# Kernel tuning notes

Measured on AMD Instinct MI355X. Metric: run time of the kernel, lower is better.

Reference implementation:

```python
import jax, jax.numpy as jnp
import numpy as np

NUM_GRAPHS = 128
N_NODES = 50000
N_EDGES = 400000
EMB = 384
L = 5
BN_EPS = 1e-5


def _bn(h, gamma, beta):
    # training-mode BatchNorm1d over the node/edge dim (biased variance, like torch)
    m = h.mean(axis=0)
    v = h.var(axis=0)
    return gamma * (h - m) * jax.lax.rsqrt(v + BN_EPS) + beta


def setup_inputs() -> dict:
    key = jax.random.key(0)
    ks = jax.random.split(key, 16)
    batch = jnp.sort(jax.random.randint(ks[0], (N_NODES,), 0, NUM_GRAPHS))
    x = jax.random.randint(ks[1], (N_NODES, 9), 0, 64)
    edge_index = jax.random.randint(ks[2], (2, N_EDGES), 0, N_NODES)
    edge_attr = jax.random.randint(ks[3], (N_EDGES, 3), 0, 8)
    s = 0.05
    atom_emb = jax.random.normal(ks[4], (9, 64, EMB), jnp.float32) * s
    bond_emb = jax.random.normal(ks[5], (3, 8, EMB), jnp.float32) * s
    # per-layer GINE MLP params, stacked over layers
    W1 = jax.random.normal(ks[6], (L, EMB, 2 * EMB), jnp.float32) * (1.0 / np.sqrt(EMB))
    b1 = jnp.zeros((L, 2 * EMB), jnp.float32)
    g1 = jnp.ones((L, 2 * EMB), jnp.float32)
    be1 = jnp.zeros((L, 2 * EMB), jnp.float32)
    W2 = jax.random.normal(ks[7], (L, 2 * EMB, EMB), jnp.float32) * (1.0 / np.sqrt(2 * EMB))
    b2 = jnp.zeros((L, EMB), jnp.float32)
    # outer per-layer BatchNorm params
    gbn = jnp.ones((L, EMB), jnp.float32)
    bbn = jnp.zeros((L, EMB), jnp.float32)
    return {"batch": batch, "x": x, "edge_index": edge_index, "edge_attr": edge_attr,
            "atom_emb": atom_emb, "bond_emb": bond_emb,
            "W1": W1, "b1": b1, "g1": g1, "be1": be1,
            "W2": W2, "b2": b2, "gbn": gbn, "bbn": bbn}


def reference(batch, x, edge_index, edge_attr, atom_emb, bond_emb,
              W1, b1, g1, be1, W2, b2, gbn, bbn):
    # AtomEncoder / BondEncoder: sum of per-column embedding lookups
    h = atom_emb[jnp.arange(9), x].sum(axis=1)          # [N, EMB]
    e = bond_emb[jnp.arange(3), edge_attr].sum(axis=1)  # [E, EMB]
    src, dst = edge_index[0], edge_index[1]
    for i in range(W1.shape[0]):
        # GINEConv: sum_j relu(x_j + e_ij)  (edge_weight defaults to ones)
        msg = jax.nn.relu(h[src] + e)                                   # [E, EMB]
        agg = jax.ops.segment_sum(msg, dst, num_segments=N_NODES)      # [N, EMB]
        z = h + agg                                                     # (1+eps)*x_i + agg, eps=0
        # MLP: Linear -> BN -> ReLU -> Linear
        z = z @ W1[i] + b1[i]
        z = jax.nn.relu(_bn(z, g1[i], be1[i]))
        z = z @ W2[i] + b2[i]
        # outer BN + ReLU (drop_ratio = 0.0)
        h = jax.nn.relu(_bn(z, gbn[i], bbn[i]))
    # standard pooling: global_add_pool
    graph_emb = jax.ops.segment_sum(h, batch, num_segments=NUM_GRAPHS)  # [G, EMB]
    return graph_emb, h
```

## Files before the change

### kernel.cpp

```cpp
#include <hip/hip_runtime.h>
#include <stdint.h>

#define NN 50000
#define NE 400000
#define EMB 384
#define NH 768
#define NL 5

typedef __bf16 bf16x8_t __attribute__((ext_vector_type(8)));
typedef float  f32x4_t  __attribute__((ext_vector_type(4)));

__device__ __forceinline__ float bflo(uint32_t u){ union{uint32_t u;float f;} v; v.u = u<<16; return v.f; }
__device__ __forceinline__ float bfhi(uint32_t u){ union{uint32_t u;float f;} v; v.u = u & 0xffff0000u; return v.f; }
__device__ __forceinline__ uint16_t f2bf(float f){
  union{float f;uint32_t u;} v; v.f=f;
  uint32_t r = v.u + 0x7fffu + ((v.u>>16)&1u);
  return (uint16_t)(r>>16);
}
__device__ __forceinline__ uint32_t bfpack2(float a, float b){
  return (uint32_t)f2bf(a) | ((uint32_t)f2bf(b)<<16);
}

__global__ void hist_kernel(const int* __restrict__ dst, int* __restrict__ count){
  int i = blockIdx.x*256 + threadIdx.x;
  if (i < NE) atomicAdd(&count[dst[i]], 1);
}
__global__ void scan_block_sum(const int* __restrict__ count, int* __restrict__ bsum, int n){
  __shared__ int s[256];
  int i = blockIdx.x*256 + threadIdx.x;
  s[threadIdx.x] = (i<n) ? count[i] : 0;
  __syncthreads();
  for (int st=128; st>0; st>>=1){
    if (threadIdx.x < st) s[threadIdx.x] += s[threadIdx.x+st];
    __syncthreads();
  }
  if (threadIdx.x==0) bsum[blockIdx.x] = s[0];
}
__global__ void scan_excl_small(int* __restrict__ bsum, int nb){
  __shared__ int s[256];
  int t = threadIdx.x;
  int v = (t<nb) ? bsum[t] : 0;
  s[t] = v;
  __syncthreads();
  for (int st=1; st<256; st<<=1){
    int u = (t>=st) ? s[t-st] : 0;
    __syncthreads();
    s[t] += u;
    __syncthreads();
  }
  if (t<nb) bsum[t] = s[t] - v;
}
__global__ void scan_final(const int* __restrict__ count, const int* __restrict__ bsum,
                           int* __restrict__ rowptr, int* __restrict__ cursor, int n){
  __shared__ int s[256];
  int t = threadIdx.x;
  int i = blockIdx.x*256 + t;
  int v = (i<n) ? count[i] : 0;
  s[t] = v;
  __syncthreads();
  for (int st=1; st<256; st<<=1){
    int u = (t>=st) ? s[t-st] : 0;
    __syncthreads();
    s[t] += u;
    __syncthreads();
  }
  int off = bsum[blockIdx.x] + s[t] - v;
  if (i < n){
    rowptr[i] = off; cursor[i] = off;
    if (i == n-1) rowptr[n] = off + v;
  }
}
__global__ void scatter_kernel(const int* __restrict__ dst, const int* __restrict__ src,
                               const int* __restrict__ eattr, int* __restrict__ cursor,
                               int* __restrict__ csr_src, int* __restrict__ csr_code){
  int e = blockIdx.x*256 + threadIdx.x;
  if (e < NE){
    int p = atomicAdd(&cursor[dst[e]], 1);
    csr_src[p] = src[e];
    csr_code[p] = eattr[e*3] | (eattr[e*3+1]<<3) | (eattr[e*3+2]<<6);
  }
}

__global__ void build_bond(const float* __restrict__ bemb, uint16_t* __restrict__ bt){
  const int code = blockIdx.x;
  const int t0 = code&7, t1=(code>>3)&7, t2=code>>6;
  const int c = threadIdx.x;
  const float2 a = ((const float2*)(bemb + (size_t)( 0+t0)*EMB))[c];
  const float2 b = ((const float2*)(bemb + (size_t)( 8+t1)*EMB))[c];
  const float2 d = ((const float2*)(bemb + (size_t)(16+t2)*EMB))[c];
  ((uint32_t*)(bt + (size_t)code*EMB))[c] = bfpack2(a.x+b.x+d.x, a.y+b.y+d.y);
}

__global__ void transpose_w(const float* __restrict__ in, uint16_t* __restrict__ outp,
                            int R, int Cc){
  __shared__ float tile[32][33];
  const size_t lo = (size_t)blockIdx.z * R * Cc;
  int cb = blockIdx.x*32, rb = blockIdx.y*32;
  int r = rb + threadIdx.y, c = cb + threadIdx.x;
  if (r < R && c < Cc) tile[threadIdx.y][threadIdx.x] = in[lo + (size_t)r*Cc + c];
  __syncthreads();
  int orr = cb + threadIdx.y, occ = rb + threadIdx.x;
  if (orr < Cc && occ < R) outp[lo + (size_t)orr*R + occ] = f2bf(tile[threadIdx.x][threadIdx.y]);
}

__global__ __launch_bounds__(256) void atom_encode(
    const int* __restrict__ x, const float* __restrict__ aemb,
    uint16_t* __restrict__ h){
  const int w = threadIdx.x >> 6, lane = threadIdx.x & 63;
  const int i = blockIdx.x*4 + w;
  if (i >= NN) return;
  float a0=0,a1=0,a2=0,a3=0,a4=0,a5=0;
  #pragma unroll
  for (int k=0;k<9;k++){
    const int idx = x[i*9+k];
    const float2* p = (const float2*)(aemb + ((size_t)(k*64+idx))*EMB) + lane*3;
    float2 u0=p[0], u1=p[1], u2=p[2];
    a0+=u0.x; a1+=u0.y; a2+=u1.x; a3+=u1.y; a4+=u2.x; a5+=u2.y;
  }
  uint32_t* hp = (uint32_t*)(h + (size_t)i*EMB) + lane*3;
  hp[0]=bfpack2(a0,a1); hp[1]=bfpack2(a2,a3); hp[2]=bfpack2(a4,a5);
}

template<int BNREL>
__global__ __launch_bounds__(256) void agg_kernel(
    const uint16_t* __restrict__ in, const uint16_t* __restrict__ bondt,
    const float* __restrict__ scale, const float* __restrict__ shift,
    const int* __restrict__ rowptr, const int* __restrict__ csr_src,
    const int* __restrict__ csr_code, uint16_t* __restrict__ za){
  const int w = threadIdx.x >> 6, lane = threadIdx.x & 63;
  const int i = blockIdx.x*4 + w;
  if (i >= NN) return;

  float sc0=0,sc1=0,sc2=0,sc3=0,sc4=0,sc5=0, sh0=0,sh1=0,sh2=0,sh3=0,sh4=0,sh5=0;
  if (BNREL){
    const int c = lane*6;
    sc0=scale[c]; sc1=scale[c+1]; sc2=scale[c+2]; sc3=scale[c+3]; sc4=scale[c+4]; sc5=scale[c+5];
    sh0=shift[c]; sh1=shift[c+1]; sh2=shift[c+2]; sh3=shift[c+3]; sh4=shift[c+4]; sh5=shift[c+5];
  }

  const uint32_t* hs = (const uint32_t*)(in + (size_t)i*EMB) + lane*3;
  uint32_t s0=hs[0], s1=hs[1], s2=hs[2];
  float a0,a1,a2,a3,a4,a5;
  if (BNREL){
    a0 = fmaxf(bflo(s0)*sc0+sh0, 0.f); a1 = fmaxf(bfhi(s0)*sc1+sh1, 0.f);
    a2 = fmaxf(bflo(s1)*sc2+sh2, 0.f); a3 = fmaxf(bfhi(s1)*sc3+sh3, 0.f);
    a4 = fmaxf(bflo(s2)*sc4+sh4, 0.f); a5 = fmaxf(bfhi(s2)*sc5+sh5, 0.f);
  } else {
    a0 = bflo(s0); a1 = bfhi(s0); a2 = bflo(s1); a3 = bfhi(s1); a4 = bflo(s2); a5 = bfhi(s2);
  }

  const int rs = rowptr[i], re = rowptr[i+1];
  int k = rs;
  for (; k + 4 <= re; k += 4){
    int sj[4], cj[4];
    #pragma unroll
    for (int j=0;j<4;j++){ sj[j]=csr_src[k+j]; cj[j]=csr_code[k+j]; }
    uint32_t u[4][3], b[4][3];
    #pragma unroll
    for (int j=0;j<4;j++){
      const uint32_t* hp = (const uint32_t*)(in + (size_t)sj[j]*EMB) + lane*3;
      u[j][0]=hp[0]; u[j][1]=hp[1]; u[j][2]=hp[2];
      const uint32_t* bp = (const uint32_t*)(bondt + (size_t)cj[j]*EMB) + lane*3;
      b[j][0]=bp[0]; b[j][1]=bp[1]; b[j][2]=bp[2];
    }
    #pragma unroll
    for (int j=0;j<4;j++){
      float v0,v1,v2,v3,v4,v5;
      if (BNREL){
        v0 = fmaxf(bflo(u[j][0])*sc0+sh0, 0.f); v1 = fmaxf(bfhi(u[j][0])*sc1+sh1, 0.f);
        v2 = fmaxf(bflo(u[j][1])*sc2+sh2, 0.f); v3 = fmaxf(bfhi(u[j][1])*sc3+sh3, 0.f);
        v4 = fmaxf(bflo(u[j][2])*sc4+sh4, 0.f); v5 = fmaxf(bfhi(u[j][2])*sc5+sh5, 0.f);
      } else {
        v0=bflo(u[j][0]); v1=bfhi(u[j][0]); v2=bflo(u[j][1]);
        v3=bfhi(u[j][1]); v4=bflo(u[j][2]); v5=bfhi(u[j][2]);
      }
      a0 += fmaxf(v0+bflo(b[j][0]), 0.f); a1 += fmaxf(v1+bfhi(b[j][0]), 0.f);
      a2 += fmaxf(v2+bflo(b[j][1]), 0.f); a3 += fmaxf(v3+bfhi(b[j][1]), 0.f);
      a4 += fmaxf(v4+bflo(b[j][2]), 0.f); a5 += fmaxf(v5+bfhi(b[j][2]), 0.f);
    }
  }
  for (; k < re; k++){
    const int s = csr_src[k];
    const int code = csr_code[k];
    const uint32_t* hp = (const uint32_t*)(in + (size_t)s*EMB) + lane*3;
    uint32_t u0=hp[0], u1=hp[1], u2=hp[2];
    const uint32_t* bp = (const uint32_t*)(bondt + (size_t)code*EMB) + lane*3;
    uint32_t b0=bp[0], b1=bp[1], b2=bp[2];
    float v0,v1,v2,v3,v4,v5;
    if (BNREL){
      v0 = fmaxf(bflo(u0)*sc0+sh0, 0.f); v1 = fmaxf(bfhi(u0)*sc1+sh1, 0.f);
      v2 = fmaxf(bflo(u1)*sc2+sh2, 0.f); v3 = fmaxf(bfhi(u1)*sc3+sh3, 0.f);
      v4 = fmaxf(bflo(u2)*sc4+sh4, 0.f); v5 = fmaxf(bfhi(u2)*sc5+sh5, 0.f);
    } else {
      v0=bflo(u0); v1=bfhi(u0); v2=bflo(u1); v3=bfhi(u1); v4=bflo(u2); v5=bfhi(u2);
    }
    a0 += fmaxf(v0+bflo(b0), 0.f); a1 += fmaxf(v1+bfhi(b0), 0.f);
    a2 += fmaxf(v2+bflo(b1), 0.f); a3 += fmaxf(v3+bfhi(b1), 0.f);
    a4 += fmaxf(v4+bflo(b2), 0.f); a5 += fmaxf(v5+bfhi(b2), 0.f);
  }

  uint32_t* zp = (uint32_t*)(za + (size_t)i*EMB) + lane*3;
  zp[0] = bfpack2(a0,a1);
  zp[1] = bfpack2(a2,a3);
  zp[2] = bfpack2(a4,a5);
}

template<int BNA>
__global__ __launch_bounds__(256) void gemm_bt(
    const uint16_t* __restrict__ A, const uint16_t* __restrict__ Bt,
    const float* __restrict__ bias, const float* __restrict__ scA,
    const float* __restrict__ shA, uint16_t* __restrict__ C,
    float* __restrict__ stats, int M, int N, int K, int nbr){
  __shared__ __align__(16) uint16_t As[128*32];
  __shared__ __align__(16) uint16_t Bs[128*32];
  __shared__ float sAs[BNA ? NH : 1];
  __shared__ float hAs[BNA ? NH : 1];
  __shared__ float csum[128];
  __shared__ float csq[128];

  const int tid = threadIdx.x;
  const int nbc = N >> 7;
  const int xcd = blockIdx.x & 7;
  const int slot = blockIdx.x >> 3;
  const int bcol = slot % nbc;
  const int brow = (slot / nbc)*8 + xcd;
  if (brow >= nbr) return;
  const int rowbase = brow << 7;

  const int lane = tid & 63;
  const int w = tid >> 6;
  const int wm = w >> 1, wn = w & 1;
  const int quad = lane >> 4, l16 = lane & 15;

  const int s0 = tid, s1 = 256 + tid;
  const int kq0 = s0 >> 7, r0 = s0 & 127;
  const int kq1 = s1 >> 7, r1 = s1 & 127;
  int gra0 = rowbase + r0; if (gra0 >= M) gra0 = M-1;
  int gra1 = rowbase + r1; if (gra1 >= M) gra1 = M-1;
  const int pb0 = bcol*128 + (r0 & 64) + ((r0 & 15) << 2) + ((r0 >> 4) & 3);
  const int pb1 = bcol*128 + (r1 & 64) + ((r1 & 15) << 2) + ((r1 >> 4) & 3);

  const uint16_t* gA0 = A + (size_t)gra0*K + kq0*8;
  const uint16_t* gA1 = A + (size_t)gra1*K + kq1*8;
  const uint16_t* gB0 = Bt + (size_t)pb0*K + kq0*8;
  const uint16_t* gB1 = Bt + (size_t)pb1*K + kq1*8;

  uint4 pa0 = *(const uint4*)gA0;
  uint4 pa1 = *(const uint4*)gA1;
  uint4 pb0r = *(const uint4*)gB0;
  uint4 pb1r = *(const uint4*)gB1;
  uint4 qa0 = *(const uint4*)(gA0 + 32);
  uint4 qa1 = *(const uint4*)(gA1 + 32);
  uint4 qb0r = *(const uint4*)(gB0 + 32);
  uint4 qb1r = *(const uint4*)(gB1 + 32);

  if (BNA){
    for (int i = tid; i < K; i += 256){ sAs[i] = scA[i]; hAs[i] = shA[i]; }
    __syncthreads();
  }

  f32x4_t acc[4][4];
  #pragma unroll
  for (int mi=0;mi<4;mi++)
    #pragma unroll
    for (int ni=0;ni<4;ni++)
      acc[mi][ni] = (f32x4_t){0.f,0.f,0.f,0.f};

  for (int k0 = 0; k0 < K; k0 += 64){
    if (!BNA){
      *(uint4*)&As[s0*8] = pa0;
      *(uint4*)&As[s1*8] = pa1;
    } else {
      uint32_t in0[4] = {pa0.x,pa0.y,pa0.z,pa0.w};
      uint32_t in1[4] = {pa1.x,pa1.y,pa1.z,pa1.w};
      uint32_t o0[4], o1[4];
      const int kb0 = k0 + kq0*8, kb1 = k0 + kq1*8;
      #pragma unroll
      for (int j=0;j<4;j++){
        float x0 = fmaxf(bflo(in0[j])*sAs[kb0+2*j  ]+hAs[kb0+2*j  ], 0.f);
        float x1 = fmaxf(bfhi(in0[j])*sAs[kb0+2*j+1]+hAs[kb0+2*j+1], 0.f);
        o0[j] = bfpack2(x0,x1);
        float y0 = fmaxf(bflo(in1[j])*sAs[kb1+2*j  ]+hAs[kb1+2*j  ], 0.f);
        float y1 = fmaxf(bfhi(in1[j])*sAs[kb1+2*j+1]+hAs[kb1+2*j+1], 0.f);
        o1[j] = bfpack2(y0,y1);
      }
      *(uint4*)&As[s0*8] = make_uint4(o0[0],o0[1],o0[2],o0[3]);
      *(uint4*)&As[s1*8] = make_uint4(o1[0],o1[1],o1[2],o1[3]);
    }
    *(uint4*)&Bs[s0*8] = pb0r;
    *(uint4*)&Bs[s1*8] = pb1r;
    __syncthreads();

    if (k0 + 64 < K){
      const int kn = k0 + 64;
      pa0 = *(const uint4*)(gA0 + kn);
      pa1 = *(const uint4*)(gA1 + kn);
      pb0r = *(const uint4*)(gB0 + kn);
      pb1r = *(const uint4*)(gB1 + kn);
    }

    {
      bf16x8_t fa[4], fb[4];
      #pragma unroll
      for (int mi=0;mi<4;mi++)
        fa[mi] = *(const bf16x8_t*)&As[(quad*128 + wm*64 + mi*16 + l16)*8];
      #pragma unroll
      for (int ni=0;ni<4;ni++)
        fb[ni] = *(const bf16x8_t*)&Bs[(quad*128 + wn*64 + ni*16 + l16)*8];
      #pragma unroll
      for (int mi=0;mi<4;mi++)
        #pragma unroll
        for (int ni=0;ni<4;ni++)
          acc[mi][ni] = __builtin_amdgcn_mfma_f32_16x16x32_bf16(fa[mi], fb[ni], acc[mi][ni], 0,0,0);
    }
    __syncthreads();

    if (!BNA){
      *(uint4*)&As[s0*8] = qa0;
      *(uint4*)&As[s1*8] = qa1;
    } else {
      uint32_t in0[4] = {qa0.x,qa0.y,qa0.z,qa0.w};
      uint32_t in1[4] = {qa1.x,qa1.y,qa1.z,qa1.w};
      uint32_t o0[4], o1[4];
      const int kb0 = k0 + 32 + kq0*8, kb1 = k0 + 32 + kq1*8;
      #pragma unroll
      for (int j=0;j<4;j++){
        float x0 = fmaxf(bflo(in0[j])*sAs[kb0+2*j  ]+hAs[kb0+2*j  ], 0.f);
        float x1 = fmaxf(bfhi(in0[j])*sAs[kb0+2*j+1]+hAs[kb0+2*j+1], 0.f);
        o0[j] = bfpack2(x0,x1);
        float y0 = fmaxf(bflo(in1[j])*sAs[kb1+2*j  ]+hAs[kb1+2*j  ], 0.f);
        float y1 = fmaxf(bfhi(in1[j])*sAs[kb1+2*j+1]+hAs[kb1+2*j+1], 0.f);
        o1[j] = bfpack2(y0,y1);
      }
      *(uint4*)&As[s0*8] = make_uint4(o0[0],o0[1],o0[2],o0[3]);
      *(uint4*)&As[s1*8] = make_uint4(o1[0],o1[1],o1[2],o1[3]);
    }
    *(uint4*)&Bs[s0*8] = qb0r;
    *(uint4*)&Bs[s1*8] = qb1r;
    __syncthreads();

    if (k0 + 96 < K){
      const int kn = k0 + 96;
      qa0 = *(const uint4*)(gA0 + kn);
      qa1 = *(const uint4*)(gA1 + kn);
      qb0r = *(const uint4*)(gB0 + kn);
      qb1r = *(const uint4*)(gB1 + kn);
    }

    {
      bf16x8_t fa[4], fb[4];
      #pragma unroll
      for (int mi=0;mi<4;mi++)
        fa[mi] = *(const bf16x8_t*)&As[(quad*128 + wm*64 + mi*16 + l16)*8];
      #pragma unroll
      for (int ni=0;ni<4;ni++)
        fb[ni] = *(const bf16x8_t*)&Bs[(quad*128 + wn*64 + ni*16 + l16)*8];
      #pragma unroll
      for (int mi=0;mi<4;mi++)
        #pragma unroll
        for (int ni=0;ni<4;ni++)
          acc[mi][ni] = __builtin_amdgcn_mfma_f32_16x16x32_bf16(fa[mi], fb[ni], acc[mi][ni], 0,0,0);
    }
    __syncthreads();
  }

  if (tid < 128){ csum[tid]=0.f; csq[tid]=0.f; }
  __syncthreads();

  const int lcol = wn*64 + l16*4;
  const int colbase = bcol*128 + lcol;
  float bv[4], ssum[4] = {0,0,0,0}, sq[4] = {0,0,0,0};
  #pragma unroll
  for (int ni=0;ni<4;ni++) bv[ni] = bias[colbase + ni];

  #pragma unroll
  for (int mi=0;mi<4;mi++){
    #pragma unroll
    for (int r=0;r<4;r++){
      const int grow = rowbase + wm*64 + mi*16 + quad*4 + r;
      if (grow < M){
        float v0 = acc[mi][0][r] + bv[0];
        float v1 = acc[mi][1][r] + bv[1];
        float v2 = acc[mi][2][r] + bv[2];
        float v3 = acc[mi][3][r] + bv[3];
        uint2 pk = make_uint2(bfpack2(v0,v1), bfpack2(v2,v3));
        *(uint2*)(C + (size_t)grow*N + colbase) = pk;
        ssum[0]+=v0; ssum[1]+=v1; ssum[2]+=v2; ssum[3]+=v3;
        sq[0]+=v0*v0; sq[1]+=v1*v1; sq[2]+=v2*v2; sq[3]+=v3*v3;
      }
    }
  }
  #pragma unroll
  for (int ni=0;ni<4;ni++){
    ssum[ni] += __shfl_xor(ssum[ni], 16); ssum[ni] += __shfl_xor(ssum[ni], 32);
    sq[ni]   += __shfl_xor(sq[ni],   16); sq[ni]   += __shfl_xor(sq[ni],   32);
  }
  if (quad == 0){
    #pragma unroll
    for (int ni=0;ni<4;ni++){
      atomicAdd(&csum[lcol + ni], ssum[ni]);
      atomicAdd(&csq [lcol + ni], sq[ni]);
    }
  }
  __syncthreads();
  if (tid < 128){
    atomicAdd(&stats[bcol*128 + tid], csum[tid]);
    atomicAdd(&stats[N + bcol*128 + tid], csq[tid]);
  }
}

__global__ void bn_finalize(float* __restrict__ stats, const float* __restrict__ gamma,
                            const float* __restrict__ beta, float* __restrict__ scale,
                            float* __restrict__ shift, int n, float invM){
  int c = blockIdx.x*256 + threadIdx.x;
  if (c < n){
    float mean = stats[c]*invM;
    float var  = stats[n+c]*invM - mean*mean;
    float sc = gamma[c] * rsqrtf(var + 1e-5f);
    scale[c] = sc;
    shift[c] = beta[c] - mean*sc;
    stats[c] = 0.f;
    stats[n+c] = 0.f;
  }
}

__global__ void bn_relu_final(const uint16_t* __restrict__ u, const float* __restrict__ scale,
                              const float* __restrict__ shift, float* __restrict__ hf){
  int i = blockIdx.x*256 + threadIdx.x;
  const int total2 = NN*EMB/2;
  if (i >= total2) return;
  uint32_t v = ((const uint32_t*)u)[i];
  int c = (i*2) % EMB;
  float f0 = fmaxf(bflo(v)*scale[c  ] + shift[c  ], 0.f);
  float f1 = fmaxf(bfhi(v)*scale[c+1] + shift[c+1], 0.f);
  ((float2*)hf)[i] = make_float2(f0, f1);
}

__global__ void pool_kernel(const float* __restrict__ h, const int* __restrict__ batch,
                            float* __restrict__ pool){
  __shared__ int bs[64];
  int c = threadIdx.x;
  int n0 = blockIdx.x*64;
  if (c < 64){ int i = n0 + c; bs[c] = (i < NN) ? batch[i] : -1; }
  __syncthreads();
  float sum = 0.f; int cur = -1;
  for (int tt=0; tt<64; tt++){
    int i = n0 + tt;
    if (i >= NN) break;
    int g = bs[tt];
    float v = h[(size_t)i*EMB + c];
    if (g != cur){
      if (cur >= 0) atomicAdd(&pool[(size_t)cur*EMB + c], sum);
      cur = g; sum = v;
    } else sum += v;
  }
  if (cur >= 0) atomicAdd(&pool[(size_t)cur*EMB + c], sum);
}
__global__ void pool_to_out(const float* __restrict__ pool, float* __restrict__ outp){
  int i = blockIdx.x*256 + threadIdx.x;
  if (i < 128*EMB) outp[i] = pool[i];
}

extern "C" void kernel_launch(void* const* d_in, const int* in_sizes, int n_in,
                              void* d_out, int out_size, void* d_ws, size_t ws_size,
                              hipStream_t stream){
  (void)in_sizes; (void)n_in; (void)out_size; (void)ws_size;
  const int* batch = (const int*)d_in[0];
  const int* x     = (const int*)d_in[1];
  const int* eidx  = (const int*)d_in[2];
  const int* eattr = (const int*)d_in[3];
  const float* aemb = (const float*)d_in[4];
  const float* bemb = (const float*)d_in[5];
  const float* W1 = (const float*)d_in[6];
  const float* b1 = (const float*)d_in[7];
  const float* g1 = (const float*)d_in[8];
  const float* be1= (const float*)d_in[9];
  const float* W2 = (const float*)d_in[10];
  const float* b2 = (const float*)d_in[11];
  const float* gbn= (const float*)d_in[12];
  const float* bbn= (const float*)d_in[13];
  float* out = (float*)d_out;

  char* base = (char*)d_ws;
  size_t off = 0;
  auto alloc = [&](size_t bytes) -> void* {
    void* p = base + off;
    off = (off + bytes + 255) & ~(size_t)255;
    return p;
  };
  uint16_t* za   = (uint16_t*)alloc((size_t)NN*EMB*2);
  uint16_t* zm   = (uint16_t*)alloc((size_t)NN*EMB*2);
  uint16_t* t    = (uint16_t*)alloc((size_t)NN*NH*2);
  uint16_t* W1t  = (uint16_t*)alloc((size_t)NL*NH*EMB*2);
  uint16_t* W2t  = (uint16_t*)alloc((size_t)NL*EMB*NH*2);
  uint16_t* bondt= (uint16_t*)alloc((size_t)512*EMB*2);
  float* stats1  = (float*)alloc(NH*2*4);
  float* stats2  = (float*)alloc(EMB*2*4);
  float* scale1  = (float*)alloc(NH*4);
  float* shift1  = (float*)alloc(NH*4);
  float* scale2  = (float*)alloc(EMB*4);
  float* shift2  = (float*)alloc(EMB*4);
  float* pool    = (float*)alloc(128*EMB*4);
  int* count   = (int*)alloc((size_t)NN*4);
  int* rowptr  = (int*)alloc((size_t)(NN+1)*4);
  int* cursor  = (int*)alloc((size_t)NN*4);
  int* bsum    = (int*)alloc(256*4);
  int* csr_src = (int*)alloc((size_t)NE*4);
  int* csr_code= (int*)alloc((size_t)NE*4);

  const int* esrc = eidx;
  const int* edst = eidx + NE;
  const int nsb = (NN + 255)/256;

  hipMemsetAsync(count, 0, (size_t)NN*4, stream);
  hist_kernel<<<(NE+255)/256, 256, 0, stream>>>(edst, count);
  scan_block_sum<<<nsb, 256, 0, stream>>>(count, bsum, NN);
  scan_excl_small<<<1, 256, 0, stream>>>(bsum, nsb);
  scan_final<<<nsb, 256, 0, stream>>>(count, bsum, rowptr, cursor, NN);
  scatter_kernel<<<(NE+255)/256, 256, 0, stream>>>(edst, esrc, eattr, cursor, csr_src, csr_code);

  build_bond<<<512, 192, 0, stream>>>(bemb, bondt);
  transpose_w<<<dim3(NH/32, EMB/32, NL), dim3(32,32), 0, stream>>>(W1, W1t, EMB, NH);
  transpose_w<<<dim3(EMB/32, NH/32, NL), dim3(32,32), 0, stream>>>(W2, W2t, NH, EMB);

  atom_encode<<<NN/4, 256, 0, stream>>>(x, aemb, zm);
  hipMemsetAsync(pool, 0, (size_t)128*EMB*4, stream);
  hipMemsetAsync(stats1, 0, (size_t)(6144 + 3072), stream);

  const int nbr = (NN + 127)/128;
  const int nbrr = ((nbr + 7)/8)*8;
  const int g1blocks = nbrr*(NH/128);
  const int g2blocks = nbrr*(EMB/128);
  for (int l = 0; l < NL; l++){
    if (l == 0)
      agg_kernel<0><<<NN/4, 256, 0, stream>>>(zm, bondt, nullptr, nullptr,
                                              rowptr, csr_src, csr_code, za);
    else
      agg_kernel<1><<<NN/4, 256, 0, stream>>>(zm, bondt, scale2, shift2,
                                              rowptr, csr_src, csr_code, za);
    gemm_bt<0><<<g1blocks, 256, 0, stream>>>(
        za, W1t + (size_t)l*NH*EMB, b1 + l*NH, nullptr, nullptr, t, stats1, NN, NH, EMB, nbr);
    bn_finalize<<<(NH+255)/256, 256, 0, stream>>>(stats1, g1 + l*NH, be1 + l*NH,
                                                  scale1, shift1, NH, 1.0f/NN);
    gemm_bt<1><<<g2blocks, 256, 0, stream>>>(
        t, W2t + (size_t)l*EMB*NH, b2 + l*EMB, scale1, shift1, zm, stats2, NN, EMB, NH, nbr);
    bn_finalize<<<(EMB+255)/256, 256, 0, stream>>>(stats2, gbn + l*EMB, bbn + l*EMB,
                                                   scale2, shift2, EMB, 1.0f/NN);
  }
  bn_relu_final<<<(NN*EMB/2 + 255)/256, 256, 0, stream>>>(zm, scale2, shift2, out + 128*EMB);
  pool_kernel<<<(NN+63)/64, 384, 0, stream>>>(out + 128*EMB, batch, pool);
  pool_to_out<<<(128*EMB+255)/256, 256, 0, stream>>>(pool, out);
}
```

Before: 1.302 ms.

## Double-buffer GEMM LDS tiles and load via direct global-to-LDS DMA

The GEMM main loop now uses two LDS buffers for A and B. It uses global_load_lds to stream B tiles, and A tiles when no BN prologue is needed, straight into the next buffer while MFMAs run on the current one. This removes the register staging round trip and one of the two barriers per k-step. The BN-fused A path still goes through registers and is written into the alternate buffer. The change doubles LDS use, which may reduce occupancy. It also depends on the direct-to-LDS loads being complete by the barrier, with no explicit wait on vmcnt.

```diff
diff --git a/kernel.cpp b/kernel.cpp
--- a/kernel.cpp
+++ b/kernel.cpp
@@ -19,6 +19,13 @@
 }
 __device__ __forceinline__ uint32_t bfpack2(float a, float b){
   return (uint32_t)f2bf(a) | ((uint32_t)f2bf(b)<<16);
+}
+
+__device__ __forceinline__ void gld16(uint16_t* ldsp, const uint16_t* gp){
+  __builtin_amdgcn_global_load_lds(
+      (const __attribute__((address_space(1))) uint32_t*)gp,
+      (__attribute__((address_space(3))) uint32_t*)ldsp,
+      16, 0, 0);
 }
 
 __global__ void hist_kernel(const int* __restrict__ dst, int* __restrict__ count){
@@ -211,8 +218,8 @@
     const float* __restrict__ bias, const float* __restrict__ scA,
     const float* __restrict__ shA, uint16_t* __restrict__ C,
     float* __restrict__ stats, int M, int N, int K, int nbr){
-  __shared__ __align__(16) uint16_t As[128*32];
-  __shared__ __align__(16) uint16_t Bs[128*32];
+  __shared__ __align__(16) uint16_t As[2][128*32];
+  __shared__ __align__(16) uint16_t Bs[2][128*32];
   __shared__ float sAs[BNA ? NH : 1];
   __shared__ float hAs[BNA ? NH : 1];
   __shared__ float csum[128];
@@ -245,20 +252,6 @@
   const uint16_t* gB0 = Bt + (size_t)pb0*K + kq0*8;
   const uint16_t* gB1 = Bt + (size_t)pb1*K + kq1*8;
 
-  uint4 pa0 = *(const uint4*)gA0;
-  uint4 pa1 = *(const uint4*)gA1;
-  uint4 pb0r = *(const uint4*)gB0;
-  uint4 pb1r = *(const uint4*)gB1;
-  uint4 qa0 = *(const uint4*)(gA0 + 32);
-  uint4 qa1 = *(const uint4*)(gA1 + 32);
-  uint4 qb0r = *(const uint4*)(gB0 + 32);
-  uint4 qb1r = *(const uint4*)(gB1 + 32);
-
-  if (BNA){
-    for (int i = tid; i < K; i += 256){ sAs[i] = scA[i]; hAs[i] = shA[i]; }
-    __syncthreads();
-  }
-
   f32x4_t acc[4][4];
   #pragma unroll
   for (int mi=0;mi<4;mi++)
@@ -266,102 +259,94 @@
     for (int ni=0;ni<4;ni++)
       acc[mi][ni] = (f32x4_t){0.f,0.f,0.f,0.f};
 
-  for (int k0 = 0; k0 < K; k0 += 64){
-    if (!BNA){
-      *(uint4*)&As[s0*8] = pa0;
-      *(uint4*)&As[s1*8] = pa1;
-    } else {
-      uint32_t in0[4] = {pa0.x,pa0.y,pa0.z,pa0.w};
-      uint32_t in1[4] = {pa1.x,pa1.y,pa1.z,pa1.w};
-      uint32_t o0[4], o1[4];
-      const int kb0 = k0 + kq0*8, kb1 = k0 + kq1*8;
-      #pragma unroll
-      for (int j=0;j<4;j++){
-        float x0 = fmaxf(bflo(in0[j])*sAs[kb0+2*j  ]+hAs[kb0+2*j  ], 0.f);
-        float x1 = fmaxf(bfhi(in0[j])*sAs[kb0+2*j+1]+hAs[kb0+2*j+1], 0.f);
-        o0[j] = bfpack2(x0,x1);
-        float y0 = fmaxf(bflo(in1[j])*sAs[kb1+2*j  ]+hAs[kb1+2*j  ], 0.f);
-        float y1 = fmaxf(bfhi(in1[j])*sAs[kb1+2*j+1]+hAs[kb1+2*j+1], 0.f);
-        o1[j] = bfpack2(y0,y1);
-      }
-      *(uint4*)&As[s0*8] = make_uint4(o0[0],o0[1],o0[2],o0[3]);
-      *(uint4*)&As[s1*8] = make_uint4(o1[0],o1[1],o1[2],o1[3]);
-    }
-    *(uint4*)&Bs[s0*8] = pb0r;
-    *(uint4*)&Bs[s1*8] = pb1r;
-    __syncthreads();
-
-    if (k0 + 64 < K){
-      const int kn = k0 + 64;
-      pa0 = *(const uint4*)(gA0 + kn);
-      pa1 = *(const uint4*)(gA1 + kn);
-      pb0r = *(const uint4*)(gB0 + kn);
-      pb1r = *(const uint4*)(gB1 + kn);
-    }
-
-    {
-      bf16x8_t fa[4], fb[4];
-      #pragma unroll
-      for (int mi=0;mi<4;mi++)
-        fa[mi] = *(const bf16x8_t*)&As[(quad*128 + wm*64 + mi*16 + l16)*8];
+  auto stageB = [&](int buf, int kk){
+    gld16(&Bs[buf][s0*8], gB0 + kk);
+    gld16(&Bs[buf][s1*8], gB1 + kk);
+  };
+  auto stageA_dma = [&](int buf, int kk){
+    gld16(&As[buf][s0*8], gA0 + kk);
+    gld16(&As[buf][s1*8], gA1 + kk);
+  };
+  auto stageA_bn = [&](int buf, int kk, uint4 va, uint4 vb){
+    uint32_t in0[4] = {va.x,va.y,va.z,va.w};
+    uint32_t in1[4] = {vb.x,vb.y,vb.z,vb.w};
+    uint32_t o0[4], o1[4];
+    const int kb0 = kk + kq0*8, kb1 = kk + kq1*8;
+    #pragma unroll
+    for (int j=0;j<4;j++){
+      float x0 = fmaxf(bflo(in0[j])*sAs[kb0+2*j  ]+hAs[kb0+2*j  ], 0.f);
+      float x1 = fmaxf(bfhi(in0[j])*sAs[kb0+2*j+1]+hAs[kb0+2*j+1], 0.f);
+      o0[j] = bfpack2(x0,x1);
+      float y0 = fmaxf(bflo(in1[j])*sAs[kb1+2*j  ]+hAs[kb1+2*j  ], 0.f);
+      float y1 = fmaxf(bfhi(in1[j])*sAs[kb1+2*j+1]+hAs[kb1+2*j+1], 0.f);
+      o1[j] = bfpack2(y0,y1);
+    }
+    *(uint4*)&As[buf][s0*8] = make_uint4(o0[0],o0[1],o0[2],o0[3]);
+    *(uint4*)&As[buf][s1*8] = make_uint4(o1[0],o1[1],o1[2],o1[3]);
+  };
+  auto compute = [&](int buf){
+    bf16x8_t fa[4], fb[4];
+    #pragma unroll
+    for (int mi=0;mi<4;mi++)
+      fa[mi] = *(const bf16x8_t*)&As[buf][(quad*128 + wm*64 + mi*16 + l16)*8];
+    #pragma unroll
+    for (int ni=0;ni<4;ni++)
+      fb[ni] = *(const bf16x8_t*)&Bs[buf][(quad*128 + wn*64 + ni*16 + l16)*8];
+    #pragma unroll
+    for (int mi=0;mi<4;mi++)
       #pragma unroll
       for (int ni=0;ni<4;ni++)
-        fb[ni] = *(const bf16x8_t*)&Bs[(quad*128 + wn*64 + ni*16 + l16)*8];
-      #pragma unroll
-      for (int mi=0;mi<4;mi++)
-        #pragma unroll
-        for (int ni=0;ni<4;ni++)
-          acc[mi][ni] = __builtin_amdgcn_mfma_f32_16x16x32_bf16(fa[mi], fb[ni], acc[mi][ni], 0,0,0);
-    }
+        acc[mi][ni] = __builtin_amdgcn_mfma_f32_16x16x32_bf16(fa[mi], fb[ni], acc[mi][ni], 0,0,0);
+  };
+
+  const int nk = K >> 5;
+
+  uint4 pa0{}, pa1{}, qa0{}, qa1{};
+  if (BNA){
+    for (int i = tid; i < K; i += 256){ sAs[i] = scA[i]; hAs[i] = shA[i]; }
+    pa0 = *(const uint4*)(gA0);      pa1 = *(const uint4*)(gA1);
+    qa0 = *(const uint4*)(gA0 + 32); qa1 = *(const uint4*)(gA1 + 32);
     __syncthreads();
-
-    if (!BNA){
-      *(uint4*)&As[s0*8] = qa0;
-      *(uint4*)&As[s1*8] = qa1;
-    } else {
-      uint32_t in0[4] = {qa0.x,qa0.y,qa0.z,qa0.w};
-      uint32_t in1[4] = {qa1.x,qa1.y,qa1.z,qa1.w};
-      uint32_t o0[4], o1[4];
-      const int kb0 = k0 + 32 + kq0*8, kb1 = k0 + 32 + kq1*8;
-      #pragma unroll
-      for (int j=0;j<4;j++){
-        float x0 = fmaxf(bflo(in0[j])*sAs[kb0+2*j  ]+hAs[kb0+2*j  ], 0.f);
-        float x1 = fmaxf(bfhi(in0[j])*sAs[kb0+2*j+1]+hAs[kb0+2*j+1], 0.f);
-        o0[j] = bfpack2(x0,x1);
-        float y0 = fmaxf(bflo(in1[j])*sAs[kb1+2*j  ]+hAs[kb1+2*j  ], 0.f);
-        float y1 = fmaxf(bfhi(in1[j])*sAs[kb1+2*j+1]+hAs[kb1+2*j+1], 0.f);
-        o1[j] = bfpack2(y0,y1);
+    stageA_bn(0, 0, pa0, pa1);
+    if (nk > 2){ pa0 = *(const uint4*)(gA0 + 64); pa1 = *(const uint4*)(gA1 + 64); }
+  } else {
+    stageA_dma(0, 0);
+  }
+  stageB(0, 0);
+  __syncthreads();
+
+  int cur = 0;
+  for (int ks = 0; ks < nk; ks += 2){
+    {
+      const int nx = cur ^ 1;
+      if (ks + 1 < nk){
+        stageB(nx, (ks+1)*32);
+        if (BNA) stageA_bn(nx, (ks+1)*32, qa0, qa1);
+        else     stageA_dma(nx, (ks+1)*32);
       }
-      *(uint4*)&As[s0*8] = make_uint4(o0[0],o0[1],o0[2],o0[3]);
-      *(uint4*)&As[s1*8] = make_uint4(o1[0],o1[1],o1[2],o1[3]);
-    }
-    *(uint4*)&Bs[s0*8] = qb0r;
-    *(uint4*)&Bs[s1*8] = qb1r;
-    __syncthreads();
-
-    if (k0 + 96 < K){
-      const int kn = k0 + 96;
-      qa0 = *(const uint4*)(gA0 + kn);
-      qa1 = *(const uint4*)(gA1 + kn);
-      qb0r = *(const uint4*)(gB0 + kn);
-      qb1r = *(const uint4*)(gB1 + kn);
-    }
-
+      if (BNA && ks + 3 < nk){
+        qa0 = *(const uint4*)(gA0 + (ks+3)*32);
+        qa1 = *(const uint4*)(gA1 + (ks+3)*32);
+      }
+      compute(cur);
+      __syncthreads();
+      cur = nx;
+    }
     {
-      bf16x8_t fa[4], fb[4];
-      #pragma unroll
-      for (int mi=0;mi<4;mi++)
-        fa[mi] = *(const bf16x8_t*)&As[(quad*128 + wm*64 + mi*16 + l16)*8];
-      #pragma unroll
-      for (int ni=0;ni<4;ni++)
-        fb[ni] = *(const bf16x8_t*)&Bs[(quad*128 + wn*64 + ni*16 + l16)*8];
-      #pragma unroll
-      for (int mi=0;mi<4;mi++)
-        #pragma unroll
-        for (int ni=0;ni<4;ni++)
-          acc[mi][ni] = __builtin_amdgcn_mfma_f32_16x16x32_bf16(fa[mi], fb[ni], acc[mi][ni], 0,0,0);
-    }
-    __syncthreads();
+      const int nx = cur ^ 1;
+      if (ks + 2 < nk){
+        stageB(nx, (ks+2)*32);
+        if (BNA) stageA_bn(nx, (ks+2)*32, pa0, pa1);
+        else     stageA_dma(nx, (ks+2)*32);
+      }
+      if (BNA && ks + 4 < nk){
+        pa0 = *(const uint4*)(gA0 + (ks+4)*32);
+        pa1 = *(const uint4*)(gA1 + (ks+4)*32);
+      }
+      compute(cur);
+      __syncthreads();
+      cur = nx;
+    }
   }
 
   if (tid < 128){ csum[tid]=0.f; csq[tid]=0.f; }
```

Result: no change. 1.320 ms (+1.4%).
